# Kernel tuning notes

Measured on AMD Instinct MI355X. Metric: run time of the kernel, lower is better.

## Reference

```python
import jax, jax.numpy as jnp
import numpy as np

B, N, HID = 2, 512, 768
BIAF = 256
CLS = 14
CH = 32
SIZE_DIM = 25
N_POS = 30
HSZ = 2 * (BIAF + 1) + SIZE_DIM


def setup_inputs() -> dict:
    key = jax.random.key(0)
    ks = jax.random.split(key, 16)
    s = 0.02
    return {
        "x": jax.random.normal(ks[0], (B, N, HID), jnp.float32),
        "y": jax.random.normal(ks[1], (B, N, HID), jnp.float32),
        "z": jax.random.normal(ks[2], (B, N, N, CH), jnp.float32),
        "mlp1_w": jax.random.normal(ks[3], (BIAF, HID), jnp.float32) * s,
        "mlp1_b": jnp.zeros((BIAF,), jnp.float32),
        "mlp2_w": jax.random.normal(ks[4], (BIAF, HID), jnp.float32) * s,
        "mlp2_b": jnp.zeros((BIAF,), jnp.float32),
        "head_w": jax.random.normal(ks[5], (BIAF, HID), jnp.float32) * s,
        "head_b": jnp.zeros((BIAF,), jnp.float32),
        "tail_w": jax.random.normal(ks[6], (BIAF, HID), jnp.float32) * s,
        "tail_b": jnp.zeros((BIAF,), jnp.float32),
        "biaf_W": jax.random.normal(ks[7], (CLS, BIAF + 1, BIAF + 1), jnp.float32) * s,
        "W": jax.random.normal(ks[8], (CLS, HSZ), jnp.float32) * s,
        "size_emb": jax.random.normal(ks[9], (N_POS, SIZE_DIM), jnp.float32) * s,
    }


def reference(x, y, z, mlp1_w, mlp1_b, mlp2_w, mlp2_b, head_w, head_b,
              tail_w, tail_b, biaf_W, W, size_emb):
    # MLP branches (dropout=0 at eval; torch GELU is exact erf)
    h = jax.nn.gelu(x @ mlp1_w.T + mlp1_b, approximate=False)   # (b,m,BIAF)
    t = jax.nn.gelu(y @ mlp2_w.T + mlp2_b, approximate=False)   # (b,n,BIAF)
    ones = jnp.ones(h.shape[:-1] + (1,), h.dtype)
    h1 = jnp.concatenate([h, ones], -1)                          # (b,m,BIAF+1)
    t1 = jnp.concatenate([t, ones], -1)                          # (b,n,BIAF+1)
    # Biaffine with bias_x=bias_y=True -> (b,cls,m,n)
    o1 = jnp.einsum('bmi,kij,bnj->bkmn', h1, biaf_W, t1)

    # head/tail MLPs with LeakyReLU(0.01), then append 1-column
    head = jax.nn.leaky_relu(x @ head_w.T + head_b, 0.01)
    tail = jax.nn.leaky_relu(x @ tail_w.T + tail_b, 0.01)
    head = jnp.concatenate([head, ones], -1)                     # (b,m,BIAF+1)
    tail = jnp.concatenate([tail, ones], -1)                     # (b,n,BIAF+1)

    # einsum('bmnh,kh->bkmn', cat([head_m, tail_n, size_mn]), W) decomposed so
    # the (b,m,n,HSZ) pairwise tensor is never materialized (same math).
    d = head.shape[-1]
    Wh, Wt, Ws = W[:, :d], W[:, d:2 * d], W[:, 2 * d:]
    n = x.shape[1]
    ar = jnp.arange(n)
    ids = jnp.clip(ar[None, :] - ar[:, None], -N_POS // 2, N_POS // 2 - 1) + N_POS // 2
    se = size_emb[ids]                                           # (m,n,SIZE_DIM)
    o3 = (jnp.einsum('bmh,kh->bkm', head, Wh)[:, :, :, None]
          + jnp.einsum('bnh,kh->bkn', tail, Wt)[:, :, None, :]
          + jnp.einsum('mnh,kh->kmn', se, Ws)[None])
    return o1 + o3
```

## Files before the change

kernel.cpp:

```cpp
#include <hip/hip_runtime.h>
#include <hip/hip_bf16.h>
#include <math.h>
#include <stdint.h>

#define BDIM 2
#define NDIM 512
#define HID 768
#define BIAF 256
#define CLS 14
#define DD 257
#define NPOS 30
#define SDIM 25
#define HSZ 539
#define PK 288
#define PJ 384

typedef unsigned short ushort_t;
typedef __attribute__((ext_vector_type(8))) short short8;
typedef __attribute__((ext_vector_type(4))) float floatx4;

#define MFMA16(a, b, c) __builtin_amdgcn_mfma_f32_16x16x32_bf16((a), (b), (c), 0, 0, 0)

__device__ inline float bf2f(ushort_t u) {
    union { unsigned int i; float f; } c; c.i = ((unsigned)u) << 16; return c.f;
}
__device__ inline ushort_t f2bf(float f) {
    __hip_bfloat16 h = __float2bfloat16(f);
    return *(ushort_t*)&h;
}

__device__ inline void glds16(const ushort_t* g, const ushort_t* l) {
    __builtin_amdgcn_global_load_lds(
        (const __attribute__((address_space(1))) unsigned int*)(unsigned long long)(uintptr_t)g,
        (__attribute__((address_space(3))) unsigned int*)(unsigned int)(uintptr_t)l,
        16, 0, 0);
}

__global__ __launch_bounds__(256) void repack_t(
    const float* __restrict__ biafW, ushort_t* __restrict__ packW)
{
    __shared__ float tile[32][33];
    const int i0 = blockIdx.x * 32;
    const int j0 = blockIdx.y * 32;
    const int k  = blockIdx.z;
    const int r8 = threadIdx.x >> 5;
    const int c  = threadIdx.x & 31;
    #pragma unroll
    for (int rr = 0; rr < 4; ++rr) {
        int r = rr * 8 + r8;
        int gi = i0 + r, gj = j0 + c;
        tile[r][c] = (gi < DD && gj < DD) ? biafW[((size_t)k * DD + gi) * DD + gj] : 0.f;
    }
    __syncthreads();
    #pragma unroll
    for (int rr = 0; rr < 4; ++rr) {
        int jr = rr * 8 + r8;
        packW[((size_t)k * PJ + (j0 + jr)) * PK + i0 + c] = f2bf(tile[c][jr]);
    }
}

__global__ __launch_bounds__(256) void wsplit(
    const float* __restrict__ m1w, const float* __restrict__ m2w,
    const float* __restrict__ hw,  const float* __restrict__ tw,
    ushort_t* __restrict__ whi, ushort_t* __restrict__ wlo)
{
    int idx = blockIdx.x * 256 + threadIdx.x;
    int mat = idx / (BIAF * HID);
    int rem = idx % (BIAF * HID);
    const float* src = (mat == 0) ? m1w : (mat == 1) ? m2w : (mat == 2) ? hw : tw;
    float v = src[rem];
    ushort_t h = f2bf(v);
    whi[idx] = h;
    wlo[idx] = f2bf(v - bf2f(h));
}

__global__ __launch_bounds__(256) void xysplit(
    const float* __restrict__ x, const float* __restrict__ y,
    ushort_t* __restrict__ xhi, ushort_t* __restrict__ xlo,
    ushort_t* __restrict__ yhi, ushort_t* __restrict__ ylo)
{
    int idx = blockIdx.x * 256 + threadIdx.x;
    int which = idx >= (BDIM*NDIM*HID);
    int rem = which ? idx - BDIM*NDIM*HID : idx;
    float v = (which ? y : x)[rem];
    ushort_t h = f2bf(v);
    (which ? yhi : xhi)[rem] = h;
    (which ? ylo : xlo)[rem] = f2bf(v - bf2f(h));
}

__global__ void fill_pads(ushort_t* __restrict__ h1hi, ushort_t* __restrict__ h1lo,
                          ushort_t* __restrict__ t1hi, ushort_t* __restrict__ t1lo) {
    int idx = blockIdx.x * 256 + threadIdx.x;
    int plane = idx >> 15;
    int tok = (idx >> 5) & 1023;
    int c   = 256 + (idx & 31);
    ushort_t* dst = (plane == 0) ? h1hi : (plane == 1) ? h1lo : (plane == 2) ? t1hi : t1lo;
    ushort_t val = (c == 256 && (plane == 0 || plane == 2)) ? (ushort_t)0x3F80 : (ushort_t)0;
    dst[(size_t)tok * PK + c] = val;
}

__global__ __launch_bounds__(256) void proj_mfma(
    const ushort_t* __restrict__ xhi, const ushort_t* __restrict__ xlo,
    const ushort_t* __restrict__ yhi, const ushort_t* __restrict__ ylo,
    const ushort_t* __restrict__ whi, const ushort_t* __restrict__ wlo,
    const float* __restrict__ m1b, const float* __restrict__ m2b,
    const float* __restrict__ hb,  const float* __restrict__ tb,
    ushort_t* __restrict__ h1hi, ushort_t* __restrict__ h1lo,
    ushort_t* __restrict__ t1hi, ushort_t* __restrict__ t1lo,
    float* __restrict__ headf, float* __restrict__ tailf)
{
    const int ft = blockIdx.x;
    const int mt = blockIdx.y;
    const int proj = blockIdx.z;
    const int wave = threadIdx.x >> 6, L = threadIdx.x & 63;
    const int quad = L >> 4, l16 = L & 15;
    const int tok0 = mt * 64 + wave * 16;
    const int f0 = ft * 32;

    const ushort_t* ahi_p = (proj == 1) ? yhi : xhi;
    const ushort_t* alo_p = (proj == 1) ? ylo : xlo;
    const float* bias = (proj == 0) ? m1b : (proj == 1) ? m2b : (proj == 2) ? hb : tb;

    const size_t aoff = (size_t)(tok0 + l16) * HID + quad * 8;
    const size_t wbase = (size_t)proj * BIAF * HID;
    const size_t b0 = wbase + (size_t)(f0 + l16) * HID + quad * 8;
    const size_t b1 = wbase + (size_t)(f0 + 16 + l16) * HID + quad * 8;

    floatx4 acc0 = {0.f, 0.f, 0.f, 0.f}, acc1 = {0.f, 0.f, 0.f, 0.f};
    #pragma unroll 4
    for (int k0 = 0; k0 < HID; k0 += 32) {
        short8 ah  = *(const short8*)(ahi_p + aoff + k0);
        short8 al  = *(const short8*)(alo_p + aoff + k0);
        short8 bh0 = *(const short8*)(whi + b0 + k0);
        short8 bl0 = *(const short8*)(wlo + b0 + k0);
        short8 bh1 = *(const short8*)(whi + b1 + k0);
        short8 bl1 = *(const short8*)(wlo + b1 + k0);
        acc0 = MFMA16(ah, bh0, acc0);
        acc1 = MFMA16(ah, bh1, acc1);
        acc0 = MFMA16(al, bh0, acc0);
        acc1 = MFMA16(al, bh1, acc1);
        acc0 = MFMA16(ah, bl0, acc0);
        acc1 = MFMA16(ah, bl1, acc1);
    }

    #pragma unroll
    for (int nf = 0; nf < 2; ++nf) {
        floatx4 a = nf ? acc1 : acc0;
        int feat = f0 + nf * 16 + l16;
        float bv = bias[feat];
        #pragma unroll
        for (int r = 0; r < 4; ++r) {
            int tok = tok0 + quad * 4 + r;
            float v = a[r] + bv;
            if (proj <= 1) {
                float g = 0.5f * v * (1.0f + erff(v * 0.70710678118654752f));
                ushort_t h = f2bf(g);
                ushort_t lo = f2bf(g - bf2f(h));
                if (proj == 0) { h1hi[(size_t)tok * PK + feat] = h; h1lo[(size_t)tok * PK + feat] = lo; }
                else           { t1hi[(size_t)tok * PK + feat] = h; t1lo[(size_t)tok * PK + feat] = lo; }
            } else {
                float lv = (v >= 0.f) ? v : 0.01f * v;
                if (proj == 2) headf[(size_t)tok * 256 + feat] = lv;
                else           tailf[(size_t)tok * 256 + feat] = lv;
            }
        }
    }
}

__global__ __launch_bounds__(256) void hk_tk_kernel(
    const float* __restrict__ headf, const float* __restrict__ tailf,
    const float* __restrict__ W,
    float* __restrict__ hk, float* __restrict__ tk)
{
    int p = blockIdx.x * 256 + threadIdx.x;
    int which = p >> 14;
    int idx = p & 16383;
    int tok = idx >> 4;
    int k = idx & 15;
    if (k >= CLS) return;
    const float* row = (which ? tailf : headf) + (size_t)tok * 256;
    const float* wr = W + (size_t)k * HSZ + (which ? DD : 0);
    float acc = 0.f;
    for (int f4 = 0; f4 < 64; ++f4) {
        float4 rv = *(const float4*)(row + f4 * 4);
        acc += rv.x * wr[f4*4] + rv.y * wr[f4*4+1] + rv.z * wr[f4*4+2] + rv.w * wr[f4*4+3];
    }
    acc += wr[256];
    float* dst = which ? tk : hk;
    dst[(size_t)(tok >> 9) * CLS * NDIM + (size_t)k * NDIM + (tok & 511)] = acc;
}

__global__ void sk_kernel(const float* __restrict__ semb, const float* __restrict__ W,
                          float* __restrict__ sk)
{
    int idx = blockIdx.x * 256 + threadIdx.x;
    if (idx < CLS * NPOS) {
        int k = idx / NPOS, d = idx % NPOS;
        float acc = 0.f;
        for (int h = 0; h < SDIM; ++h)
            acc += semb[d*SDIM + h] * W[k*HSZ + 2*DD + h];
        sk[idx] = acc;
    }
}

__global__ __launch_bounds__(256) void mb_tile(
    const ushort_t* __restrict__ h1hi, const ushort_t* __restrict__ h1lo,
    const ushort_t* __restrict__ packW,
    ushort_t* __restrict__ Ab)
{
    __shared__ ushort_t Ah[64 * 32];
    __shared__ ushort_t Al[64 * 32];
    __shared__ ushort_t Bt[96 * 32];
    const int jt = blockIdx.x, mt = blockIdx.y, bk = blockIdx.z;
    const int b = bk / CLS, k = bk % CLS;
    const int tid = threadIdx.x;
    const int wave = tid >> 6, L = tid & 63;
    const int quad = L >> 4, l16 = L & 15;
    const int lrow = L >> 2, lq = L & 3;
    const int m0 = mt * 64, j0 = jt * 96;
    const int wm = (wave >> 1) * 32, wj = (wave & 1) * 48;

    const ushort_t* gAh = h1hi + (size_t)(b * NDIM + m0) * PK;
    const ushort_t* gAl = h1lo + (size_t)(b * NDIM + m0) * PK;
    const ushort_t* gB  = packW + ((size_t)k * PJ + j0) * PK;

    floatx4 acc[2][3];
    #pragma unroll
    for (int mi = 0; mi < 2; ++mi)
        #pragma unroll
        for (int ni = 0; ni < 3; ++ni)
            #pragma unroll
            for (int r = 0; r < 4; ++r) acc[mi][ni][r] = 0.f;

    for (int k0 = 0; k0 < PK; k0 += 32) {
        for (int s = wave; s < 14; s += 4) {
            const ushort_t* g; const ushort_t* l;
            if (s < 4)      { l = Ah + s * 512;       g = gAh + (size_t)(s * 16 + lrow) * PK + k0 + lq * 8; }
            else if (s < 8) { l = Al + (s - 4) * 512; g = gAl + (size_t)((s - 4) * 16 + lrow) * PK + k0 + lq * 8; }
            else            { l = Bt + (s - 8) * 512; g = gB  + (size_t)((s - 8) * 16 + lrow) * PK + k0 + lq * 8; }
            glds16(g, l);
        }
        __syncthreads();
        short8 ah[2], al[2], bb[3];
        #pragma unroll
        for (int mi = 0; mi < 2; ++mi) {
            ah[mi] = *(const short8*)(Ah + (wm + mi * 16 + l16) * 32 + quad * 8);
            al[mi] = *(const short8*)(Al + (wm + mi * 16 + l16) * 32 + quad * 8);
        }
        #pragma unroll
        for (int ni = 0; ni < 3; ++ni)
            bb[ni] = *(const short8*)(Bt + (wj + ni * 16 + l16) * 32 + quad * 8);
        #pragma unroll
        for (int mi = 0; mi < 2; ++mi)
            #pragma unroll
            for (int ni = 0; ni < 3; ++ni) {
                acc[mi][ni] = MFMA16(ah[mi], bb[ni], acc[mi][ni]);
                acc[mi][ni] = MFMA16(al[mi], bb[ni], acc[mi][ni]);
            }
        __syncthreads();
    }

    ushort_t* Aout = Ab + (size_t)bk * NDIM * PK;
    #pragma unroll
    for (int mi = 0; mi < 2; ++mi) {
        #pragma unroll
        for (int r = 0; r < 4; ++r) {
            int row = m0 + wm + mi * 16 + quad * 4 + r;
            #pragma unroll
            for (int ni = 0; ni < 3; ++ni) {
                int col = j0 + wj + ni * 16 + l16;
                Aout[(size_t)row * PK + col] = f2bf(acc[mi][ni][r]);
            }
        }
    }
}

__global__ __launch_bounds__(256) void mo_tile(
    const ushort_t* __restrict__ Ab,
    const ushort_t* __restrict__ t1hi, const ushort_t* __restrict__ t1lo,
    const float* __restrict__ hk, const float* __restrict__ tk,
    const float* __restrict__ sk,
    float* __restrict__ out)
{
    __shared__ ushort_t At[64 * 32];
    __shared__ ushort_t Bh[128 * 32];
    __shared__ ushort_t Bl[128 * 32];
    __shared__ float skr[NPOS];
    const int nt = blockIdx.x, mt = blockIdx.y, bk = blockIdx.z;
    const int b = bk / CLS, k = bk % CLS;
    const int tid = threadIdx.x;
    if (tid < NPOS) skr[tid] = sk[k * NPOS + tid];
    const int wave = tid >> 6, L = tid & 63;
    const int quad = L >> 4, l16 = L & 15;
    const int lrow = L >> 2, lq = L & 3;
    const int m0 = mt * 64, n0 = nt * 128;
    const int wm = (wave >> 1) * 32, wn = (wave & 1) * 64;

    const ushort_t* gA  = Ab + ((size_t)bk * NDIM + m0) * PK;
    const ushort_t* gBh = t1hi + (size_t)(b * NDIM + n0) * PK;
    const ushort_t* gBl = t1lo + (size_t)(b * NDIM + n0) * PK;

    floatx4 acc[2][4];
    #pragma unroll
    for (int mi = 0; mi < 2; ++mi)
        #pragma unroll
        for (int ni = 0; ni < 4; ++ni)
            #pragma unroll
            for (int r = 0; r < 4; ++r) acc[mi][ni][r] = 0.f;

    for (int k0 = 0; k0 < PK; k0 += 32) {
        for (int s = wave; s < 20; s += 4) {
            const ushort_t* g; const ushort_t* l;
            if (s < 4)       { l = At + s * 512;        g = gA  + (size_t)(s * 16 + lrow) * PK + k0 + lq * 8; }
            else if (s < 12) { l = Bh + (s - 4) * 512;  g = gBh + (size_t)((s - 4) * 16 + lrow) * PK + k0 + lq * 8; }
            else             { l = Bl + (s - 12) * 512; g = gBl + (size_t)((s - 12) * 16 + lrow) * PK + k0 + lq * 8; }
            glds16(g, l);
        }
        __syncthreads();
        short8 a[2], bh[4], bl[4];
        #pragma unroll
        for (int mi = 0; mi < 2; ++mi)
            a[mi] = *(const short8*)(At + (wm + mi * 16 + l16) * 32 + quad * 8);
        #pragma unroll
        for (int ni = 0; ni < 4; ++ni) {
            bh[ni] = *(const short8*)(Bh + (wn + ni * 16 + l16) * 32 + quad * 8);
            bl[ni] = *(const short8*)(Bl + (wn + ni * 16 + l16) * 32 + quad * 8);
        }
        #pragma unroll
        for (int mi = 0; mi < 2; ++mi)
            #pragma unroll
            for (int ni = 0; ni < 4; ++ni) {
                acc[mi][ni] = MFMA16(a[mi], bh[ni], acc[mi][ni]);
                acc[mi][ni] = MFMA16(a[mi], bl[ni], acc[mi][ni]);
            }
        __syncthreads();
    }

    const size_t obase = (size_t)bk * NDIM;
    #pragma unroll
    for (int mi = 0; mi < 2; ++mi) {
        #pragma unroll
        for (int r = 0; r < 4; ++r) {
            int row = m0 + wm + mi * 16 + quad * 4 + r;
            float hv = hk[obase + row];
            #pragma unroll
            for (int ni = 0; ni < 4; ++ni) {
                int col = n0 + wn + ni * 16 + l16;
                int d = col - row; d = d < -15 ? -15 : (d > 14 ? 14 : d); d += 15;
                out[(obase + row) * NDIM + col] = acc[mi][ni][r] + hv + tk[obase + col] + skr[d];
            }
        }
    }
}

extern "C" void kernel_launch(void* const* d_in, const int* in_sizes, int n_in,
                              void* d_out, int out_size, void* d_ws, size_t ws_size,
                              hipStream_t stream) {
    const float* x    = (const float*)d_in[0];
    const float* y    = (const float*)d_in[1];
    const float* m1w  = (const float*)d_in[3];
    const float* m1b  = (const float*)d_in[4];
    const float* m2w  = (const float*)d_in[5];
    const float* m2b  = (const float*)d_in[6];
    const float* hw   = (const float*)d_in[7];
    const float* hb   = (const float*)d_in[8];
    const float* tw   = (const float*)d_in[9];
    const float* tb   = (const float*)d_in[10];
    const float* biafW= (const float*)d_in[11];
    const float* W    = (const float*)d_in[12];
    const float* semb = (const float*)d_in[13];

    char* p = (char*)d_ws;
    float* hk   = (float*)p;                    p += 57344;
    float* tk   = (float*)p;                    p += 57344;
    float* skp  = (float*)p;                    p += 2048;
    float* headf= (float*)p;                    p += 1048576;
    float* tailf= (float*)p;                    p += 1048576;
    ushort_t* h1hi = (ushort_t*)p;              p += 589824;
    ushort_t* h1lo = (ushort_t*)p;              p += 589824;
    ushort_t* t1hi = (ushort_t*)p;              p += 589824;
    ushort_t* t1lo = (ushort_t*)p;              p += 589824;
    ushort_t* packW= (ushort_t*)p;              p += 3096576;
    ushort_t* whi  = (ushort_t*)p;              p += 1572864;
    ushort_t* wlo  = (ushort_t*)p;              p += 1572864;
    ushort_t* Abuf = (ushort_t*)p;              p += 8257536;
    ushort_t* xhi  = (ushort_t*)p;              p += 1572864;
    ushort_t* xlo  = (ushort_t*)p;              p += 1572864;
    ushort_t* yhi  = (ushort_t*)p;              p += 1572864;
    ushort_t* ylo  = (ushort_t*)p;              p += 1572864;

    repack_t<<<dim3(9, 12, CLS), 256, 0, stream>>>(biafW, packW);
    wsplit<<<3072, 256, 0, stream>>>(m1w, m2w, hw, tw, whi, wlo);
    xysplit<<<6144, 256, 0, stream>>>(x, y, xhi, xlo, yhi, ylo);
    fill_pads<<<512, 256, 0, stream>>>(h1hi, h1lo, t1hi, t1lo);
    proj_mfma<<<dim3(8, 16, 4), 256, 0, stream>>>(xhi, xlo, yhi, ylo, whi, wlo,
                                                  m1b, m2b, hb, tb,
                                                  h1hi, h1lo, t1hi, t1lo, headf, tailf);
    hk_tk_kernel<<<128, 256, 0, stream>>>(headf, tailf, W, hk, tk);
    sk_kernel<<<2, 256, 0, stream>>>(semb, W, skp);
    mb_tile<<<dim3(3, 8, BDIM*CLS), 256, 0, stream>>>(h1hi, h1lo, packW, Abuf);
    mo_tile<<<dim3(4, 8, BDIM*CLS), 256, 0, stream>>>(Abuf, t1hi, t1lo, hk, tk, skp,
                                                      (float*)d_out);
}
```

Measured before the change: 210.8 us.

## Swizzle LDS tile layout in GEMMs and merge small prep kernels

Changes how the mb_tile and mo_tile GEMM kernels place data in LDS. The global-to-LDS copy pattern is permuted with an XOR swizzle so that the MFMA operand reads hit different LDS banks, cutting bank conflicts. It also merges the weight, x/y and pad-fill split kernels into one kernel that converts four floats per thread, and folds sk_kernel into the hk/tk kernel. Together these cut kernel launches and vectorise the conversion passes. The swizzle has to match exactly between the store mapping and the read mapping, or the results will be wrong.

Result: faster. 204.8 us (-2.9%).

```diff
diff --git a/kernel.cpp b/kernel.cpp
--- a/kernel.cpp
+++ b/kernel.cpp
@@ -18,6 +18,7 @@
 typedef unsigned short ushort_t;
 typedef __attribute__((ext_vector_type(8))) short short8;
 typedef __attribute__((ext_vector_type(4))) float floatx4;
+typedef __attribute__((ext_vector_type(4))) unsigned short ushort4_t;
 
 #define MFMA16(a, b, c) __builtin_amdgcn_mfma_f32_16x16x32_bf16((a), (b), (c), 0, 0, 0)
 
@@ -35,6 +36,7 @@
         (__attribute__((address_space(3))) unsigned int*)(unsigned int)(uintptr_t)l,
         16, 0, 0);
 }
+
 
 __global__ __launch_bounds__(256) void repack_t(
     const float* __restrict__ biafW, ushort_t* __restrict__ packW)
@@ -59,44 +61,52 @@
     }
 }
 
-__global__ __launch_bounds__(256) void wsplit(
+__global__ __launch_bounds__(256) void prep_split(
+    const float* __restrict__ x, const float* __restrict__ y,
     const float* __restrict__ m1w, const float* __restrict__ m2w,
     const float* __restrict__ hw,  const float* __restrict__ tw,
-    ushort_t* __restrict__ whi, ushort_t* __restrict__ wlo)
-{
-    int idx = blockIdx.x * 256 + threadIdx.x;
-    int mat = idx / (BIAF * HID);
-    int rem = idx % (BIAF * HID);
-    const float* src = (mat == 0) ? m1w : (mat == 1) ? m2w : (mat == 2) ? hw : tw;
-    float v = src[rem];
-    ushort_t h = f2bf(v);
-    whi[idx] = h;
-    wlo[idx] = f2bf(v - bf2f(h));
-}
-
-__global__ __launch_bounds__(256) void xysplit(
-    const float* __restrict__ x, const float* __restrict__ y,
     ushort_t* __restrict__ xhi, ushort_t* __restrict__ xlo,
-    ushort_t* __restrict__ yhi, ushort_t* __restrict__ ylo)
-{
-    int idx = blockIdx.x * 256 + threadIdx.x;
-    int which = idx >= (BDIM*NDIM*HID);
-    int rem = which ? idx - BDIM*NDIM*HID : idx;
-    float v = (which ? y : x)[rem];
-    ushort_t h = f2bf(v);
-    (which ? yhi : xhi)[rem] = h;
-    (which ? ylo : xlo)[rem] = f2bf(v - bf2f(h));
-}
-
-__global__ void fill_pads(ushort_t* __restrict__ h1hi, ushort_t* __restrict__ h1lo,
-                          ushort_t* __restrict__ t1hi, ushort_t* __restrict__ t1lo) {
-    int idx = blockIdx.x * 256 + threadIdx.x;
-    int plane = idx >> 15;
-    int tok = (idx >> 5) & 1023;
-    int c   = 256 + (idx & 31);
-    ushort_t* dst = (plane == 0) ? h1hi : (plane == 1) ? h1lo : (plane == 2) ? t1hi : t1lo;
-    ushort_t val = (c == 256 && (plane == 0 || plane == 2)) ? (ushort_t)0x3F80 : (ushort_t)0;
-    dst[(size_t)tok * PK + c] = val;
+    ushort_t* __restrict__ yhi, ushort_t* __restrict__ ylo,
+    ushort_t* __restrict__ whi, ushort_t* __restrict__ wlo,
+    ushort_t* __restrict__ h1hi, ushort_t* __restrict__ h1lo,
+    ushort_t* __restrict__ t1hi, ushort_t* __restrict__ t1lo)
+{
+    int tg = blockIdx.x * 256 + threadIdx.x;
+    if (tg < 196608) {
+        int mat = tg / 49152;
+        int e0  = (tg % 49152) * 4;
+        const float* src = (mat == 0) ? m1w : (mat == 1) ? m2w : (mat == 2) ? hw : tw;
+        float4 v = *(const float4*)(src + e0);
+        size_t o = (size_t)mat * 196608 + e0;
+        ushort4_t h, lo;
+        h[0] = f2bf(v.x); lo[0] = f2bf(v.x - bf2f(h[0]));
+        h[1] = f2bf(v.y); lo[1] = f2bf(v.y - bf2f(h[1]));
+        h[2] = f2bf(v.z); lo[2] = f2bf(v.z - bf2f(h[2]));
+        h[3] = f2bf(v.w); lo[3] = f2bf(v.w - bf2f(h[3]));
+        *(ushort4_t*)(whi + o) = h;
+        *(ushort4_t*)(wlo + o) = lo;
+    } else if (tg < 589824) {
+        int t = tg - 196608;
+        int which = t / 196608;
+        int e0 = (t % 196608) * 4;
+        const float* src = which ? y : x;
+        float4 v = *(const float4*)(src + e0);
+        ushort4_t h, lo;
+        h[0] = f2bf(v.x); lo[0] = f2bf(v.x - bf2f(h[0]));
+        h[1] = f2bf(v.y); lo[1] = f2bf(v.y - bf2f(h[1]));
+        h[2] = f2bf(v.z); lo[2] = f2bf(v.z - bf2f(h[2]));
+        h[3] = f2bf(v.w); lo[3] = f2bf(v.w - bf2f(h[3]));
+        *(ushort4_t*)((which ? yhi : xhi) + e0) = h;
+        *(ushort4_t*)((which ? ylo : xlo) + e0) = lo;
+    } else {
+        int idx = tg - 589824;
+        int plane = idx >> 15;
+        int tok = (idx >> 5) & 1023;
+        int c   = 256 + (idx & 31);
+        ushort_t* dst = (plane == 0) ? h1hi : (plane == 1) ? h1lo : (plane == 2) ? t1hi : t1lo;
+        ushort_t val = (c == 256 && (plane == 0 || plane == 2)) ? (ushort_t)0x3F80 : (ushort_t)0;
+        dst[(size_t)tok * PK + c] = val;
+    }
 }
 
 __global__ __launch_bounds__(256) void proj_mfma(
@@ -167,11 +177,22 @@
     }
 }
 
-__global__ __launch_bounds__(256) void hk_tk_kernel(
+__global__ __launch_bounds__(256) void hk_tk_sk(
     const float* __restrict__ headf, const float* __restrict__ tailf,
-    const float* __restrict__ W,
-    float* __restrict__ hk, float* __restrict__ tk)
-{
+    const float* __restrict__ W, const float* __restrict__ semb,
+    float* __restrict__ hk, float* __restrict__ tk, float* __restrict__ skp)
+{
+    if (blockIdx.x >= 128) {
+        int idx = (blockIdx.x - 128) * 256 + threadIdx.x;
+        if (idx < CLS * NPOS) {
+            int k = idx / NPOS, d = idx % NPOS;
+            float acc = 0.f;
+            for (int h = 0; h < SDIM; ++h)
+                acc += semb[d*SDIM + h] * W[k*HSZ + 2*DD + h];
+            skp[idx] = acc;
+        }
+        return;
+    }
     int p = blockIdx.x * 256 + threadIdx.x;
     int which = p >> 14;
     int idx = p & 16383;
@@ -190,19 +211,6 @@
     dst[(size_t)(tok >> 9) * CLS * NDIM + (size_t)k * NDIM + (tok & 511)] = acc;
 }
 
-__global__ void sk_kernel(const float* __restrict__ semb, const float* __restrict__ W,
-                          float* __restrict__ sk)
-{
-    int idx = blockIdx.x * 256 + threadIdx.x;
-    if (idx < CLS * NPOS) {
-        int k = idx / NPOS, d = idx % NPOS;
-        float acc = 0.f;
-        for (int h = 0; h < SDIM; ++h)
-            acc += semb[d*SDIM + h] * W[k*HSZ + 2*DD + h];
-        sk[idx] = acc;
-    }
-}
-
 __global__ __launch_bounds__(256) void mb_tile(
     const ushort_t* __restrict__ h1hi, const ushort_t* __restrict__ h1lo,
     const ushort_t* __restrict__ packW,
@@ -216,7 +224,10 @@
     const int tid = threadIdx.x;
     const int wave = tid >> 6, L = tid & 63;
     const int quad = L >> 4, l16 = L & 15;
-    const int lrow = L >> 2, lq = L & 3;
+    const int sr = L >> 3, u = (L & 7) ^ sr;
+    const int srow = 2 * sr + (u >> 2);
+    const int scol = (u & 3) * 8;
+    const int rbase = (l16 >> 1) * 64 + ((((((l16 & 1) << 2) | quad)) ^ (l16 >> 1)) * 8);
     const int m0 = mt * 64, j0 = jt * 96;
     const int wm = (wave >> 1) * 32, wj = (wave & 1) * 48;
 
@@ -235,21 +246,21 @@
     for (int k0 = 0; k0 < PK; k0 += 32) {
         for (int s = wave; s < 14; s += 4) {
             const ushort_t* g; const ushort_t* l;
-            if (s < 4)      { l = Ah + s * 512;       g = gAh + (size_t)(s * 16 + lrow) * PK + k0 + lq * 8; }
-            else if (s < 8) { l = Al + (s - 4) * 512; g = gAl + (size_t)((s - 4) * 16 + lrow) * PK + k0 + lq * 8; }
-            else            { l = Bt + (s - 8) * 512; g = gB  + (size_t)((s - 8) * 16 + lrow) * PK + k0 + lq * 8; }
+            if (s < 4)      { l = Ah + s * 512;       g = gAh + (size_t)(s * 16 + srow) * PK + k0 + scol; }
+            else if (s < 8) { l = Al + (s - 4) * 512; g = gAl + (size_t)((s - 4) * 16 + srow) * PK + k0 + scol; }
+            else            { l = Bt + (s - 8) * 512; g = gB  + (size_t)((s - 8) * 16 + srow) * PK + k0 + scol; }
             glds16(g, l);
         }
         __syncthreads();
         short8 ah[2], al[2], bb[3];
         #pragma unroll
         for (int mi = 0; mi < 2; ++mi) {
-            ah[mi] = *(const short8*)(Ah + (wm + mi * 16 + l16) * 32 + quad * 8);
-            al[mi] = *(const short8*)(Al + (wm + mi * 16 + l16) * 32 + quad * 8);
+            ah[mi] = *(const short8*)(Ah + (wm + mi * 16) * 32 + rbase);
+            al[mi] = *(const short8*)(Al + (wm + mi * 16) * 32 + rbase);
         }
         #pragma unroll
         for (int ni = 0; ni < 3; ++ni)
-            bb[ni] = *(const short8*)(Bt + (wj + ni * 16 + l16) * 32 + quad * 8);
+            bb[ni] = *(const short8*)(Bt + (wj + ni * 16) * 32 + rbase);
         #pragma unroll
         for (int mi = 0; mi < 2; ++mi)
             #pragma unroll
@@ -292,7 +303,10 @@
     if (tid < NPOS) skr[tid] = sk[k * NPOS + tid];
     const int wave = tid >> 6, L = tid & 63;
     const int quad = L >> 4, l16 = L & 15;
-    const int lrow = L >> 2, lq = L & 3;
+    const int sr = L >> 3, u = (L & 7) ^ sr;
+    const int srow = 2 * sr + (u >> 2);
+    const int scol = (u & 3) * 8;
+    const int rbase = (l16 >> 1) * 64 + ((((((l16 & 1) << 2) | quad)) ^ (l16 >> 1)) * 8);
     const int m0 = mt * 64, n0 = nt * 128;
     const int wm = (wave >> 1) * 32, wn = (wave & 1) * 64;
 
@@ -311,20 +325,20 @@
     for (int k0 = 0; k0 < PK; k0 += 32) {
         for (int s = wave; s < 20; s += 4) {
             const ushort_t* g; const ushort_t* l;
-            if (s < 4)       { l = At + s * 512;        g = gA  + (size_t)(s * 16 + lrow) * PK + k0 + lq * 8; }
-            else if (s < 12) { l = Bh + (s - 4) * 512;  g = gBh + (size_t)((s - 4) * 16 + lrow) * PK + k0 + lq * 8; }
-            else             { l = Bl + (s - 12) * 512; g = gBl + (size_t)((s - 12) * 16 + lrow) * PK + k0 + lq * 8; }
+            if (s < 4)       { l = At + s * 512;        g = gA  + (size_t)(s * 16 + srow) * PK + k0 + scol; }
+            else if (s < 12) { l = Bh + (s - 4) * 512;  g = gBh + (size_t)((s - 4) * 16 + srow) * PK + k0 + scol; }
+            else             { l = Bl + (s - 12) * 512; g = gBl + (size_t)((s - 12) * 16 + srow) * PK + k0 + scol; }
             glds16(g, l);
         }
         __syncthreads();
         short8 a[2], bh[4], bl[4];
         #pragma unroll
         for (int mi = 0; mi < 2; ++mi)
-            a[mi] = *(const short8*)(At + (wm + mi * 16 + l16) * 32 + quad * 8);
+            a[mi] = *(const short8*)(At + (wm + mi * 16) * 32 + rbase);
         #pragma unroll
         for (int ni = 0; ni < 4; ++ni) {
-            bh[ni] = *(const short8*)(Bh + (wn + ni * 16 + l16) * 32 + quad * 8);
-            bl[ni] = *(const short8*)(Bl + (wn + ni * 16 + l16) * 32 + quad * 8);
+            bh[ni] = *(const short8*)(Bh + (wn + ni * 16) * 32 + rbase);
+            bl[ni] = *(const short8*)(Bl + (wn + ni * 16) * 32 + rbase);
         }
         #pragma unroll
         for (int mi = 0; mi < 2; ++mi)
@@ -390,14 +404,13 @@
     ushort_t* ylo  = (ushort_t*)p;              p += 1572864;
 
     repack_t<<<dim3(9, 12, CLS), 256, 0, stream>>>(biafW, packW);
-    wsplit<<<3072, 256, 0, stream>>>(m1w, m2w, hw, tw, whi, wlo);
-    xysplit<<<6144, 256, 0, stream>>>(x, y, xhi, xlo, yhi, ylo);
-    fill_pads<<<512, 256, 0, stream>>>(h1hi, h1lo, t1hi, t1lo);
+    prep_split<<<2816, 256, 0, stream>>>(x, y, m1w, m2w, hw, tw,
+                                         xhi, xlo, yhi, ylo, whi, wlo,
+                                         h1hi, h1lo, t1hi, t1lo);
     proj_mfma<<<dim3(8, 16, 4), 256, 0, stream>>>(xhi, xlo, yhi, ylo, whi, wlo,
                                                   m1b, m2b, hb, tb,
                                                   h1hi, h1lo, t1hi, t1lo, headf, tailf);
-    hk_tk_kernel<<<128, 256, 0, stream>>>(headf, tailf, W, hk, tk);
-    sk_kernel<<<2, 256, 0, stream>>>(semb, W, skp);
+    hk_tk_sk<<<130, 256, 0, stream>>>(headf, tailf, W, semb, hk, tk, skp);
     mb_tile<<<dim3(3, 8, BDIM*CLS), 256, 0, stream>>>(h1hi, h1lo, packW, Abuf);
     mo_tile<<<dim3(4, 8, BDIM*CLS), 256, 0, stream>>>(Abuf, t1hi, t1lo, hk, tk, skp,
                                                       (float*)d_out);
```
